# Kernel tuning notes

Measured on AMD Instinct MI355X. Metric: run time of the kernel, lower is better.

The kernel has to match this reference:

```python
import jax, jax.numpy as jnp
import numpy as np

B, IN = 8192, 8000
C, S, O = 16, 500, 64          # num_chunks, chunk_size, fc_repr_dim
F = C * O                       # fc_0_out_feat = 1024
E, D, T = 8, 512, 2            # num_experts, fc_task_dim, num_tasks
NC = (32, 2)                    # num_classes per task
EPS = 1e-5


def _bn(h, g, b, axis):
    # training-mode BatchNorm1d: biased variance over the batch axis
    m = h.mean(axis=axis, keepdims=True)
    v = h.var(axis=axis, keepdims=True)
    return (h - m) * jax.lax.rsqrt(v + EPS) * g + b


def _swish(x):
    return x * jax.nn.sigmoid(x)


def setup_inputs() -> dict:
    key = jax.random.key(0)
    ks = jax.random.split(key, 10)
    s = 0.02
    return {
        "x": jax.random.normal(ks[0], (B, IN), dtype=jnp.float32),
        "w0": jax.random.normal(ks[1], (C, O, S), dtype=jnp.float32) * s,
        "b0": jnp.zeros((F,), jnp.float32),
        "bn0_g": jnp.ones((F,), jnp.float32),
        "bn0_b": jnp.zeros((F,), jnp.float32),
        "gate_w": jax.random.normal(ks[2], (T, F, E), dtype=jnp.float32) * s,
        "gate_b": jnp.zeros((T, E), jnp.float32),
        "exp_w": jax.random.normal(ks[3], (E, F, D), dtype=jnp.float32) * s,
        "exp_bn_g": jnp.ones((E, D), jnp.float32),
        "exp_bn_b": jnp.zeros((E, D), jnp.float32),
        "task_w": jax.random.normal(ks[4], (T, D, D), dtype=jnp.float32) * s,
        "task_bn_g": jnp.ones((T, D), jnp.float32),
        "task_bn_b": jnp.zeros((T, D), jnp.float32),
        "fin_w_a": jax.random.normal(ks[5], (D, NC[0]), dtype=jnp.float32) * s,
        "fin_b_a": jnp.zeros((NC[0],), jnp.float32),
        "fin_w_b": jax.random.normal(ks[6], (D, NC[1]), dtype=jnp.float32) * s,
        "fin_b_b": jnp.zeros((NC[1],), jnp.float32),
    }


def reference(x, w0, b0, bn0_g, bn0_b, gate_w, gate_b, exp_w, exp_bn_g,
              exp_bn_b, task_w, task_bn_g, task_bn_b, fin_w_a, fin_b_a,
              fin_w_b, fin_b_b):
    b = x.shape[0]
    # SplitLinear: block-diagonal linear over C chunks of size S -> O each
    h0 = jnp.einsum('bcs,cos->bco', x.reshape(b, C, S), w0).reshape(b, F) + b0
    h0 = _swish(_bn(h0, bn0_g, bn0_b, axis=0))                  # [B, F]
    # per-task gates with softmax over experts
    gates = jax.nn.softmax(
        jnp.einsum('bf,tfe->tbe', h0, gate_w) + gate_b[:, None, :], axis=-1)
    # expert branches: Linear(no bias) + BN + Swish, vectorized over experts
    eh = jnp.einsum('bf,efd->bed', h0, exp_w)                   # [B, E, D]
    eh = _swish(_bn(eh, exp_bn_g, exp_bn_b, axis=0))
    # gate-weighted sum over experts, per task
    mix = jnp.einsum('tbe,bed->tbd', gates, eh)                 # [T, B, D]
    # task branches: Linear(no bias) + BN + Swish
    th = jnp.einsum('tbd,tdk->tbk', mix, task_w)
    th = _swish(_bn(th, task_bn_g[:, None, :], task_bn_b[:, None, :], axis=1))
    out_a = th[0] @ fin_w_a + fin_b_a                           # [B, 32]
    out_b = th[1] @ fin_w_b + fin_b_b                           # [B, 2]
    return jnp.concatenate([out_a, out_b], axis=1)             # [B, 34]
```

## Files before the change

### kernel.cpp

```cpp
#include <hip/hip_runtime.h>
#include <math.h>

#define B_ 8192
#define IN_ 8000
#define C_ 16
#define S_ 500
#define O_ 64
#define F_ 1024
#define E_ 8
#define D_ 512
#define T_ 2
#define OUTW 34
#define EPS_ 1e-5f

typedef __attribute__((ext_vector_type(8))) short bf16x8;
typedef __attribute__((ext_vector_type(4))) float f32x4;

__device__ __forceinline__ float swishf(float x) {
    return x / (1.0f + __expf(-x));
}

__device__ __forceinline__ unsigned short f2bf(float f) {
    union { float f; unsigned u; } c;
    c.f = f;
    unsigned r = c.u + 0x7fffu + ((c.u >> 16) & 1u);
    return (unsigned short)(r >> 16);
}
__device__ __forceinline__ float bf2f(unsigned short b) {
    union { unsigned u; float f; } c;
    c.u = ((unsigned)b) << 16;
    return c.f;
}

__device__ __forceinline__ void gld16(const void* g, void* l) {
    __builtin_amdgcn_global_load_lds(
        (const __attribute__((address_space(1))) void*)g,
        (__attribute__((address_space(3))) void*)l, 16, 0, 0);
}

__global__ __launch_bounds__(256) void k_split(const float* __restrict__ x,
                                               const float* __restrict__ w0,
                                               const float* __restrict__ b0,
                                               unsigned short* __restrict__ h0raw,
                                               float* __restrict__ psum,
                                               float* __restrict__ psq) {
    __shared__ __align__(16) unsigned short As[128 * 72];
    __shared__ __align__(16) unsigned short Bs[64 * 72];
    int tid = threadIdx.x;
    int c = blockIdx.y;
    int brow0 = blockIdx.x * 128;
    const float* xp = x + (size_t)brow0 * IN_ + c * S_;
    const float* wp = w0 + (size_t)c * O_ * S_;

    int w = tid >> 6, lane = tid & 63;
    int l15 = lane & 15, quad = lane >> 4;
    int wm = w * 32;

    f32x4 acc[2][4] = {};

    for (int k0 = 0; k0 < 512; k0 += 64) {
#pragma unroll
        for (int i = 0; i < 8; i++) {
            int li = tid + i * 256;
            int row = li >> 4, c4 = li & 15;
            int gk = k0 + c4 * 4;
            float4 v = make_float4(0.f, 0.f, 0.f, 0.f);
            if (gk + 3 < S_) v = *(const float4*)(xp + (size_t)row * IN_ + gk);
            unsigned short u[4] = { f2bf(v.x), f2bf(v.y), f2bf(v.z), f2bf(v.w) };
            *(ushort4*)&As[row * 72 + c4 * 4] = *(ushort4*)u;
        }
#pragma unroll
        for (int i = 0; i < 4; i++) {
            int li = tid + i * 256;
            int row = li >> 4, c4 = li & 15;
            int gk = k0 + c4 * 4;
            float4 v = make_float4(0.f, 0.f, 0.f, 0.f);
            if (gk + 3 < S_) v = *(const float4*)(wp + (size_t)row * S_ + gk);
            unsigned short u[4] = { f2bf(v.x), f2bf(v.y), f2bf(v.z), f2bf(v.w) };
            *(ushort4*)&Bs[row * 72 + c4 * 4] = *(ushort4*)u;
        }
        __syncthreads();
#pragma unroll
        for (int kk = 0; kk < 64; kk += 32) {
            bf16x8 af[2], wf[4];
#pragma unroll
            for (int i = 0; i < 2; i++)
                af[i] = *(const bf16x8*)&As[(wm + i * 16 + l15) * 72 + kk + quad * 8];
#pragma unroll
            for (int j = 0; j < 4; j++)
                wf[j] = *(const bf16x8*)&Bs[(j * 16 + l15) * 72 + kk + quad * 8];
#pragma unroll
            for (int i = 0; i < 2; i++)
#pragma unroll
                for (int j = 0; j < 4; j++)
                    acc[i][j] = __builtin_amdgcn_mfma_f32_16x16x32_bf16(af[i], wf[j], acc[i][j], 0, 0, 0);
        }
        __syncthreads();
    }

    int colbase = c * O_;
    float sj[4], qj[4];
#pragma unroll
    for (int j = 0; j < 4; j++) {
        int col = j * 16 + l15;
        float bb = b0[colbase + col];
        float s = 0.f, q = 0.f;
#pragma unroll
        for (int i = 0; i < 2; i++) {
#pragma unroll
            for (int reg = 0; reg < 4; reg++) {
                float v = acc[i][j][reg] + bb;
                int rl = wm + i * 16 + quad * 4 + reg;
                h0raw[(size_t)(brow0 + rl) * F_ + colbase + col] = f2bf(v);
                s += v; q += v * v;
            }
        }
        s += __shfl_down(s, 32, 64); s += __shfl_down(s, 16, 64);
        q += __shfl_down(q, 32, 64); q += __shfl_down(q, 16, 64);
        sj[j] = s; qj[j] = q;
    }
    __syncthreads();
    float* red = (float*)As;
    if (lane < 16) {
#pragma unroll
        for (int j = 0; j < 4; j++) {
            int col = j * 16 + l15;
            red[col * 4 + w] = sj[j];
            red[256 + col * 4 + w] = qj[j];
        }
    }
    __syncthreads();
    if (tid < 64) {
        float ss = red[tid * 4] + red[tid * 4 + 1] + red[tid * 4 + 2] + red[tid * 4 + 3];
        float qq = red[256 + tid * 4] + red[256 + tid * 4 + 1] + red[256 + tid * 4 + 2] + red[256 + tid * 4 + 3];
        size_t idx = (size_t)blockIdx.x * F_ + colbase + tid;
        psum[idx] = ss; psq[idx] = qq;
    }
}

__global__ __launch_bounds__(64) void k_stats_b(const float* __restrict__ psum,
                                                const float* __restrict__ psq,
                                                int N, int YS,
                                                const float* __restrict__ g,
                                                const float* __restrict__ beta,
                                                unsigned long long gslab,
                                                float* __restrict__ scale,
                                                float* __restrict__ shift,
                                                unsigned long long oslab) {
    int n = blockIdx.x * 64 + threadIdx.x;
    int z = blockIdx.z;
    float s = 0.f, q = 0.f;
    for (int y = 0; y < YS; y++) {
        size_t idx = ((size_t)(z * YS + y)) * N + n;
        s += psum[idx]; q += psq[idx];
    }
    float mean = s * (1.0f / B_);
    float var = q * (1.0f / B_) - mean * mean;
    float sc = g[z * gslab + n] * rsqrtf(var + EPS_);
    scale[z * oslab + n] = sc;
    shift[z * oslab + n] = beta[z * gslab + n] - mean * sc;
}

__global__ __launch_bounds__(256) void k_wt(const float* __restrict__ in,
                                            unsigned short* __restrict__ out,
                                            int K, int N) {
    __shared__ float t[32][33];
    int k0 = blockIdx.x * 32, n0 = blockIdx.y * 32, z = blockIdx.z;
    const float* ip = in + (size_t)z * K * N;
    unsigned short* op = out + (size_t)z * N * K;
    int tn = threadIdx.x & 31, tk = threadIdx.x >> 5;
#pragma unroll
    for (int p = 0; p < 4; p++) {
        int k = tk + p * 8;
        t[k][tn] = ip[(size_t)(k0 + k) * N + n0 + tn];
    }
    __syncthreads();
    int tk2 = threadIdx.x & 31, tn2 = threadIdx.x >> 5;
#pragma unroll
    for (int p = 0; p < 4; p++) {
        int n = tn2 + p * 8;
        op[(size_t)(n0 + n) * K + k0 + tk2] = f2bf(t[tk2][n]);
    }
}

__global__ __launch_bounds__(256) void k_bnswish_gates(const unsigned short* __restrict__ h0,
                                                       const float* __restrict__ scale,
                                                       const float* __restrict__ shift,
                                                       const float* __restrict__ gate_w,
                                                       const float* __restrict__ gate_b,
                                                       unsigned short* __restrict__ h0bf,
                                                       float* __restrict__ gates) {
    int b = blockIdx.x, tid = threadIdx.x;
    float part[16];
#pragma unroll
    for (int i = 0; i < 16; i++) part[i] = 0.f;
    const unsigned short* row = h0 + (size_t)b * F_;
    unsigned short* ob = h0bf + (size_t)b * F_;
#pragma unroll
    for (int it = 0; it < 4; it++) {
        int f = tid + it * 256;
        float v = bf2f(row[f]);
        float hv = scale[f] * v + shift[f];
        float sw = swishf(hv);
        ob[f] = f2bf(sw);
        const float* gw0 = gate_w + (size_t)f * E_;
        const float* gw1 = gate_w + (size_t)(F_ * E_) + (size_t)f * E_;
#pragma unroll
        for (int e = 0; e < E_; e++) part[e] += sw * gw0[e];
#pragma unroll
        for (int e = 0; e < E_; e++) part[8 + e] += sw * gw1[e];
    }
#pragma unroll
    for (int i = 0; i < 16; i++) {
        float v = part[i];
        for (int off = 32; off > 0; off >>= 1) v += __shfl_down(v, off, 64);
        part[i] = v;
    }
    __shared__ float red[4][16];
    __shared__ float gfin[16];
    int wave = tid >> 6, lane = tid & 63;
    if (lane == 0) {
#pragma unroll
        for (int i = 0; i < 16; i++) red[wave][i] = part[i];
    }
    __syncthreads();
    if (tid < 16) {
        float v = red[0][tid] + red[1][tid] + red[2][tid] + red[3][tid];
        int t = tid >> 3, e = tid & 7;
        gfin[tid] = v + gate_b[t * E_ + e];
    }
    __syncthreads();
    if (tid < 2) {
        float mx = -1e30f;
#pragma unroll
        for (int e = 0; e < 8; e++) mx = fmaxf(mx, gfin[tid * 8 + e]);
        float ex[8], sum = 0.f;
#pragma unroll
        for (int e = 0; e < 8; e++) { ex[e] = __expf(gfin[tid * 8 + e] - mx); sum += ex[e]; }
        float inv = 1.0f / sum;
#pragma unroll
        for (int e = 0; e < 8; e++)
            gates[(size_t)tid * (B_ * E_) + (size_t)b * E_ + e] = ex[e] * inv;
    }
}

__global__ __launch_bounds__(256) void k_gemm_bf16(const unsigned short* __restrict__ A,
                                                   unsigned long long aslab,
                                                   const unsigned short* __restrict__ Wt,
                                                   unsigned long long wslab,
                                                   unsigned short* __restrict__ C,
                                                   unsigned long long cslab, int K,
                                                   float* __restrict__ psum,
                                                   float* __restrict__ psq) {
    __shared__ __align__(16) unsigned short As[128 * 32];
    __shared__ __align__(16) unsigned short Ws[128 * 32];
    int z = blockIdx.z;
    A  += (size_t)z * aslab;
    Wt += (size_t)z * wslab;
    C  += (size_t)z * cslab;
    const int N = gridDim.y * 128;
    int row0 = blockIdx.x * 128, col0 = blockIdx.y * 128;
    int tid = threadIdx.x;
    int w = tid >> 6, lane = tid & 63;
    int l15 = lane & 15, quad = lane >> 4;

    const unsigned short* ga0 = A  + (size_t)(row0 + w * 32 + (lane >> 2)) * K + (lane & 3) * 8;
    const unsigned short* ga1 = ga0 + 16 * (size_t)K;
    const unsigned short* gw0 = Wt + (size_t)(col0 + w * 32 + (lane >> 2)) * K + (lane & 3) * 8;
    const unsigned short* gw1 = gw0 + 16 * (size_t)K;
    unsigned short* la0 = As + (w * 32) * 32;
    unsigned short* la1 = As + (w * 32 + 16) * 32;
    unsigned short* lw0 = Ws + (w * 32) * 32;
    unsigned short* lw1 = Ws + (w * 32 + 16) * 32;

    int wm = (w & 1) * 64, wn = (w >> 1) * 64;
    const unsigned short* Afr = As + (size_t)(wm + l15) * 32 + quad * 8;
    const unsigned short* Wfr = Ws + (size_t)(wn + l15) * 32 + quad * 8;

    f32x4 acc[4][4] = {};

    for (int k0 = 0; k0 < K; k0 += 32) {
        gld16(ga0 + k0, la0);
        gld16(ga1 + k0, la1);
        gld16(gw0 + k0, lw0);
        gld16(gw1 + k0, lw1);
        __syncthreads();
        bf16x8 af[4], wf[4];
#pragma unroll
        for (int i = 0; i < 4; i++) af[i] = *(const bf16x8*)(Afr + i * 16 * 32);
#pragma unroll
        for (int j = 0; j < 4; j++) wf[j] = *(const bf16x8*)(Wfr + j * 16 * 32);
#pragma unroll
        for (int i = 0; i < 4; i++)
#pragma unroll
            for (int j = 0; j < 4; j++)
                acc[i][j] = __builtin_amdgcn_mfma_f32_16x16x32_bf16(af[i], wf[j], acc[i][j], 0, 0, 0);
        __syncthreads();
    }

#pragma unroll
    for (int i = 0; i < 4; i++) {
        int r = row0 + wm + i * 16 + quad * 4;
#pragma unroll
        for (int j = 0; j < 4; j++) {
            int cc = col0 + wn + j * 16 + l15;
            unsigned short* cp = C + (size_t)r * N + cc;
#pragma unroll
            for (int reg = 0; reg < 4; reg++)
                cp[(size_t)reg * N] = f2bf(acc[i][j][reg]);
        }
    }

    float* red = (float*)As;
    float sj[4], qj[4];
#pragma unroll
    for (int j = 0; j < 4; j++) {
        float s = 0.f, q = 0.f;
#pragma unroll
        for (int i = 0; i < 4; i++)
#pragma unroll
            for (int reg = 0; reg < 4; reg++) {
                float v = acc[i][j][reg];
                s += v; q += v * v;
            }
        s += __shfl_down(s, 32, 64); s += __shfl_down(s, 16, 64);
        q += __shfl_down(q, 32, 64); q += __shfl_down(q, 16, 64);
        sj[j] = s; qj[j] = q;
    }
    if (lane < 16) {
#pragma unroll
        for (int j = 0; j < 4; j++) {
            int cib = wn + j * 16 + lane;
            red[cib * 2 + (w & 1)] = sj[j];
            red[256 + cib * 2 + (w & 1)] = qj[j];
        }
    }
    __syncthreads();
    if (tid < 128) {
        float s = red[tid * 2] + red[tid * 2 + 1];
        float q = red[256 + tid * 2] + red[256 + tid * 2 + 1];
        size_t row = (size_t)z * gridDim.x + blockIdx.x;
        psum[row * N + col0 + tid] = s;
        psq[row * N + col0 + tid] = q;
    }
}

__global__ __launch_bounds__(256) void k_mix(const unsigned short* __restrict__ eh,
                                             const float* __restrict__ scale,
                                             const float* __restrict__ shift,
                                             const float* __restrict__ gates,
                                             unsigned short* __restrict__ mix) {
    __shared__ float scl[E_ * D_], shl[E_ * D_];
    __shared__ float gl[2][2][8];
    int tid = threadIdx.x;
#pragma unroll
    for (int i = 0; i < 4; i++) {
        int li = tid + i * 256;
        ((float4*)scl)[li] = ((const float4*)scale)[li];
        ((float4*)shl)[li] = ((const float4*)shift)[li];
    }
    if (tid < 32) {
        int sub = tid >> 4, t = (tid >> 3) & 1, e = tid & 7;
        gl[sub][t][e] = gates[(size_t)t * (B_ * E_) + (size_t)(blockIdx.x * 2 + sub) * E_ + e];
    }
    __syncthreads();
    int sub = tid >> 7;
    int b = blockIdx.x * 2 + sub;
    int d0 = (tid & 127) * 4;
    float a0[4] = {0.f, 0.f, 0.f, 0.f}, a1[4] = {0.f, 0.f, 0.f, 0.f};
#pragma unroll
    for (int e = 0; e < E_; e++) {
        ushort4 u = *(const ushort4*)&eh[(size_t)b * (E_ * D_) + e * D_ + d0];
        float4 sc4 = *(const float4*)&scl[e * D_ + d0];
        float4 sh4 = *(const float4*)&shl[e * D_ + d0];
        float g0 = gl[sub][0][e], g1 = gl[sub][1][e];
        unsigned short uu[4] = { u.x, u.y, u.z, u.w };
        float scv[4] = { sc4.x, sc4.y, sc4.z, sc4.w };
        float shv[4] = { sh4.x, sh4.y, sh4.z, sh4.w };
#pragma unroll
        for (int l = 0; l < 4; l++) {
            float sw = swishf(scv[l] * bf2f(uu[l]) + shv[l]);
            a0[l] += g0 * sw;
            a1[l] += g1 * sw;
        }
    }
    unsigned short o0[4], o1[4];
#pragma unroll
    for (int l = 0; l < 4; l++) { o0[l] = f2bf(a0[l]); o1[l] = f2bf(a1[l]); }
    *(ushort4*)&mix[(size_t)b * D_ + d0] = *(ushort4*)o0;
    *(ushort4*)&mix[(size_t)(B_ * D_) + (size_t)b * D_ + d0] = *(ushort4*)o1;
}

__global__ __launch_bounds__(256) void k_final(const unsigned short* __restrict__ th,
                                               const float* __restrict__ scale,
                                               const float* __restrict__ shift,
                                               const float* __restrict__ fwa,
                                               const float* __restrict__ fba,
                                               const float* __restrict__ fwb,
                                               const float* __restrict__ fbb,
                                               float* __restrict__ out) {
    __shared__ float t0[8][D_], t1[8][D_];
    __shared__ float pb[64];
    int tid = threadIdx.x;
    int b0 = blockIdx.x * 8;
#pragma unroll
    for (int t = 0; t < 2; t++) {
#pragma unroll
        for (int i = 0; i < 4; i++) {
            int li = tid + i * 256;
            int row = li >> 7, d = (li & 127) * 4;
            ushort4 u = *(const ushort4*)&th[((size_t)t * B_ + b0 + row) * D_ + d];
            unsigned short uu[4] = { u.x, u.y, u.z, u.w };
            float* dst = t ? &t1[row][d] : &t0[row][d];
#pragma unroll
            for (int l = 0; l < 4; l++)
                dst[l] = swishf(scale[t * D_ + d + l] * bf2f(uu[l]) + shift[t * D_ + d + l]);
        }
    }
    __syncthreads();
    {
        int row = tid >> 5, col = tid & 31;
        float acc = fba[col];
        for (int d = 0; d < D_; d++) acc += t0[row][d] * fwa[d * 32 + col];
        out[(size_t)(b0 + row) * OUTW + col] = acc;
    }
    if (tid < 64) {
        int row = tid >> 3, colb = (tid >> 2) & 1, part = tid & 3;
        float a = 0.f;
        for (int d = part * 128; d < part * 128 + 128; d++) a += t1[row][d] * fwb[d * 2 + colb];
        pb[tid] = a;
    }
    __syncthreads();
    if (tid < 16) {
        int row = tid >> 1, colb = tid & 1;
        int base = row * 8 + colb * 4;
        float a = fbb[colb] + pb[base] + pb[base + 1] + pb[base + 2] + pb[base + 3];
        out[(size_t)(b0 + row) * OUTW + 32 + colb] = a;
    }
}

extern "C" void kernel_launch(void* const* d_in, const int* in_sizes, int n_in,
                              void* d_out, int out_size, void* d_ws, size_t ws_size,
                              hipStream_t stream) {
    const float* x        = (const float*)d_in[0];
    const float* w0       = (const float*)d_in[1];
    const float* b0       = (const float*)d_in[2];
    const float* bn0_g    = (const float*)d_in[3];
    const float* bn0_b    = (const float*)d_in[4];
    const float* gate_w   = (const float*)d_in[5];
    const float* gate_b   = (const float*)d_in[6];
    const float* exp_w    = (const float*)d_in[7];
    const float* exp_bn_g = (const float*)d_in[8];
    const float* exp_bn_b = (const float*)d_in[9];
    const float* task_w   = (const float*)d_in[10];
    const float* task_bn_g= (const float*)d_in[11];
    const float* task_bn_b= (const float*)d_in[12];
    const float* fwa      = (const float*)d_in[13];
    const float* fba      = (const float*)d_in[14];
    const float* fwb      = (const float*)d_in[15];
    const float* fbb      = (const float*)d_in[16];
    float* out = (float*)d_out;

    float* ws = (float*)d_ws;
    unsigned short* ehbf  = (unsigned short*)ws;
    unsigned short* h0raw = (unsigned short*)(ws + 16777216);
    unsigned short* thbf  = ehbf;
    unsigned short* mixbf = h0raw;
    unsigned short* h0bf  = (unsigned short*)(ws + 20971520);
    unsigned short* wtE   = (unsigned short*)(ws + 25165824);
    unsigned short* twt   = (unsigned short*)(ws + 27262976);
    float* gates = ws + 27525120;
    float* sc0   = ws + 27656192;
    float* sh0   = sc0 + 1024;
    float* scE   = sh0 + 1024;
    float* shE   = scE + 4096;
    float* scT   = shE + 4096;
    float* shT   = scT + 1024;
    float* psum  = shT + 1024;
    float* psq   = psum + 262144;

    k_wt<<<dim3(32, 16, 8), 256, 0, stream>>>(exp_w, wtE, F_, D_);
    k_wt<<<dim3(16, 16, 2), 256, 0, stream>>>(task_w, twt, D_, D_);
    k_split<<<dim3(64, 16), 256, 0, stream>>>(x, w0, b0, h0raw, psum, psq);
    k_stats_b<<<dim3(16, 1, 1), 64, 0, stream>>>(psum, psq, F_, 64, bn0_g, bn0_b, 0ull, sc0, sh0, 0ull);
    k_bnswish_gates<<<dim3(B_), 256, 0, stream>>>(h0raw, sc0, sh0, gate_w, gate_b, h0bf, gates);
    k_gemm_bf16<<<dim3(64, 32, 1), 256, 0, stream>>>(h0bf, 0ull, wtE, 0ull, ehbf, 0ull, F_, psum, psq);
    k_stats_b<<<dim3(64, 1, 1), 64, 0, stream>>>(psum, psq, E_ * D_, 64, exp_bn_g, exp_bn_b, 0ull, scE, shE, 0ull);
    k_mix<<<dim3(B_ / 2), 256, 0, stream>>>(ehbf, scE, shE, gates, mixbf);
    k_gemm_bf16<<<dim3(64, 4, 2), 256, 0, stream>>>(mixbf, (unsigned long long)(B_ * D_),
                                                    twt, (unsigned long long)(D_ * D_),
                                                    thbf, (unsigned long long)(B_ * D_), D_,
                                                    psum, psq);
    k_stats_b<<<dim3(8, 1, 2), 64, 0, stream>>>(psum, psq, D_, 64, task_bn_g, task_bn_b, 512ull, scT, shT, 512ull);
    k_final<<<dim3(B_ / 8), 256, 0, stream>>>(thbf, scT, shT, fwa, fba, fwb, fbb, out);
}
```

Baseline: 689.9 us.

## Add 256x256-tile ping-pong MFMA GEMM for expert projection and vectorize bnswish

Replaces the expert GEMM (8192x4096x1024) with a new 512-thread kernel that computes 256x256 output tiles. It double-buffers LDS loads, raises wave priority around MFMA phases, swizzles block order for cache locality, and fuses BN partial statistics at the new row-block granularity (32 partials). It also vectorizes the bnswish/gates kernel loads and stores to 4-wide. The goal is more data reuse per tile and fewer global loads, at the cost of heavy register pressure and only 512 blocks.

```diff
diff --git a/kernel.cpp b/kernel.cpp
--- a/kernel.cpp
+++ b/kernel.cpp
@@ -196,20 +196,26 @@
     for (int i = 0; i < 16; i++) part[i] = 0.f;
     const unsigned short* row = h0 + (size_t)b * F_;
     unsigned short* ob = h0bf + (size_t)b * F_;
-#pragma unroll
-    for (int it = 0; it < 4; it++) {
-        int f = tid + it * 256;
-        float v = bf2f(row[f]);
-        float hv = scale[f] * v + shift[f];
-        float sw = swishf(hv);
-        ob[f] = f2bf(sw);
-        const float* gw0 = gate_w + (size_t)f * E_;
-        const float* gw1 = gate_w + (size_t)(F_ * E_) + (size_t)f * E_;
+    int f0 = tid * 4;
+    ushort4 u = *(const ushort4*)(row + f0);
+    float4 sc4 = *(const float4*)(scale + f0);
+    float4 sh4 = *(const float4*)(shift + f0);
+    unsigned short uu[4] = { u.x, u.y, u.z, u.w };
+    float scv[4] = { sc4.x, sc4.y, sc4.z, sc4.w };
+    float shv[4] = { sh4.x, sh4.y, sh4.z, sh4.w };
+    unsigned short ov[4];
+#pragma unroll
+    for (int j = 0; j < 4; j++) {
+        float sw = swishf(scv[j] * bf2f(uu[j]) + shv[j]);
+        ov[j] = f2bf(sw);
+        const float* gw0 = gate_w + (size_t)(f0 + j) * E_;
+        const float* gw1 = gw0 + (size_t)F_ * E_;
 #pragma unroll
         for (int e = 0; e < E_; e++) part[e] += sw * gw0[e];
 #pragma unroll
         for (int e = 0; e < E_; e++) part[8 + e] += sw * gw1[e];
     }
+    *(ushort4*)(ob + f0) = *(ushort4*)ov;
 #pragma unroll
     for (int i = 0; i < 16; i++) {
         float v = part[i];
@@ -342,6 +348,172 @@
         size_t row = (size_t)z * gridDim.x + blockIdx.x;
         psum[row * N + col0 + tid] = s;
         psq[row * N + col0 + tid] = q;
+    }
+}
+
+__global__ __launch_bounds__(512, 2) void k_gemm256(const unsigned short* __restrict__ A,
+                                                    const unsigned short* __restrict__ Wt,
+                                                    unsigned short* __restrict__ Cc,
+                                                    int N, int K,
+                                                    float* __restrict__ psum,
+                                                    float* __restrict__ psq) {
+    __shared__ __align__(16) unsigned short lds[2][2][2][8192];
+    int tid = threadIdx.x;
+    int w = tid >> 6, lane = tid & 63;
+    int l15 = lane & 15, quad = lane >> 4;
+    int wm = w >> 2, wn = w & 3;
+
+    int lin = blockIdx.y * gridDim.x + blockIdx.x;
+    int cpx = (gridDim.x * gridDim.y) >> 3;
+    int swz = (lin & 7) * cpx + (lin >> 3);
+    int bx = swz & (gridDim.x - 1), by = swz / gridDim.x;
+    int row0 = bx * 256, col0 = by * 256;
+
+    int srow = tid >> 3, sperm = (tid & 7) ^ (srow & 7);
+    const unsigned short* pA = A  + (size_t)(row0 + srow) * K + sperm * 8;
+    const unsigned short* pB = Wt + (size_t)(col0 + srow) * K + sperm * 8;
+
+    int aoffs[2];
+#pragma unroll
+    for (int kk = 0; kk < 2; kk++)
+        aoffs[kk] = l15 * 64 + ((kk * 4 + quad) ^ (l15 & 7)) * 8;
+
+    f32x4 acc[8][4] = {};
+    bf16x8 afr[4][2], bfr[2][2];
+    int nt = K >> 6;
+
+#define STAGE256(t1, nb) do {                                                              \
+    const unsigned short* sA = pA + (size_t)(t1) * 64;                                     \
+    const unsigned short* sB = pB + (size_t)(t1) * 64;                                     \
+    _Pragma("unroll")                                                                      \
+    for (int h = 0; h < 2; h++)                                                            \
+        _Pragma("unroll")                                                                  \
+        for (int L = 0; L < 2; L++) {                                                      \
+            gld16(sA + (size_t)(h * 128 + L * 64) * K, &lds[nb][0][h][w * 512 + L * 4096]);\
+            gld16(sB + (size_t)(h * 128 + L * 64) * K, &lds[nb][1][h][w * 512 + L * 4096]);\
+        }                                                                                  \
+} while (0)
+
+#define LDA256(mh) do {                                                                    \
+    _Pragma("unroll")                                                                      \
+    for (int mf = 0; mf < 4; mf++)                                                         \
+        _Pragma("unroll")                                                                  \
+        for (int kk = 0; kk < 2; kk++)                                                     \
+            afr[mf][kk] = *(const bf16x8*)(Ab + ((mh) * 4 + mf) * 1024 + aoffs[kk]);       \
+} while (0)
+
+#define LDB256(nh) do {                                                                    \
+    _Pragma("unroll")                                                                      \
+    for (int nf = 0; nf < 2; nf++)                                                         \
+        _Pragma("unroll")                                                                  \
+        for (int kk = 0; kk < 2; kk++)                                                     \
+            bfr[nf][kk] = *(const bf16x8*)(Bb + ((nh) * 2 + nf) * 1024 + aoffs[kk]);       \
+} while (0)
+
+#define MMA256(mh, nh) do {                                                                \
+    _Pragma("unroll")                                                                      \
+    for (int mf = 0; mf < 4; mf++)                                                         \
+        _Pragma("unroll")                                                                  \
+        for (int nf = 0; nf < 2; nf++)                                                     \
+            _Pragma("unroll")                                                              \
+            for (int kk = 0; kk < 2; kk++)                                                 \
+                acc[(mh) * 4 + mf][(nh) * 2 + nf] = __builtin_amdgcn_mfma_f32_16x16x32_bf16(\
+                    afr[mf][kk], bfr[nf][kk], acc[(mh) * 4 + mf][(nh) * 2 + nf], 0, 0, 0); \
+} while (0)
+
+#define PHASE_MID()                                                                        \
+    __builtin_amdgcn_s_barrier();                                                          \
+    asm volatile("s_waitcnt lgkmcnt(0)" ::: "memory");                                     \
+    __builtin_amdgcn_sched_barrier(0);                                                     \
+    __builtin_amdgcn_s_setprio(1);
+
+#define PHASE_END()                                                                        \
+    __builtin_amdgcn_s_setprio(0);                                                         \
+    __builtin_amdgcn_sched_barrier(0);                                                     \
+    __builtin_amdgcn_s_barrier();
+
+    STAGE256(0, 0);
+    asm volatile("s_waitcnt vmcnt(0)" ::: "memory");
+    __builtin_amdgcn_s_barrier();
+
+    for (int t = 0; t < nt; t++) {
+        int buf = t & 1;
+        const unsigned short* Ab = &lds[buf][0][wm][0];
+        const unsigned short* Bb = &lds[buf][1][wn >> 1][(wn & 1) * 4096];
+        LDA256(0); LDB256(0);
+        if (t + 1 < nt) STAGE256(t + 1, buf ^ 1);
+        PHASE_MID();
+        MMA256(0, 0);
+        PHASE_END();
+        LDB256(1);
+        PHASE_MID();
+        MMA256(0, 1);
+        PHASE_END();
+        LDA256(1);
+        PHASE_MID();
+        MMA256(1, 1);
+        PHASE_END();
+        LDB256(0);
+        PHASE_MID();
+        MMA256(1, 0);
+        __builtin_amdgcn_s_setprio(0);
+        __builtin_amdgcn_sched_barrier(0);
+        asm volatile("s_waitcnt vmcnt(0)" ::: "memory");
+        __builtin_amdgcn_s_barrier();
+    }
+#undef STAGE256
+#undef LDA256
+#undef LDB256
+#undef MMA256
+#undef PHASE_MID
+#undef PHASE_END
+
+    __syncthreads();
+
+#pragma unroll
+    for (int mf = 0; mf < 8; mf++) {
+        int r = row0 + wm * 128 + mf * 16 + quad * 4;
+#pragma unroll
+        for (int nf = 0; nf < 4; nf++) {
+            int cc = col0 + wn * 64 + nf * 16 + l15;
+            unsigned short* cp = Cc + (size_t)r * N + cc;
+#pragma unroll
+            for (int reg = 0; reg < 4; reg++)
+                cp[(size_t)reg * N] = f2bf(acc[mf][nf][reg]);
+        }
+    }
+
+    float* red = (float*)&lds[0][0][0][0];
+    float* redq = red + 512;
+    float sj[4], qj[4];
+#pragma unroll
+    for (int nf = 0; nf < 4; nf++) {
+        float s = 0.f, q = 0.f;
+#pragma unroll
+        for (int mf = 0; mf < 8; mf++)
+#pragma unroll
+            for (int reg = 0; reg < 4; reg++) {
+                float v = acc[mf][nf][reg];
+                s += v; q += v * v;
+            }
+        s += __shfl_down(s, 32, 64); s += __shfl_down(s, 16, 64);
+        q += __shfl_down(q, 32, 64); q += __shfl_down(q, 16, 64);
+        sj[nf] = s; qj[nf] = q;
+    }
+    if (quad == 0) {
+#pragma unroll
+        for (int nf = 0; nf < 4; nf++) {
+            int cib = wn * 64 + nf * 16 + l15;
+            red[cib * 2 + wm] = sj[nf];
+            redq[cib * 2 + wm] = qj[nf];
+        }
+    }
+    __syncthreads();
+    if (tid < 256) {
+        float s = red[tid * 2] + red[tid * 2 + 1];
+        float q = redq[tid * 2] + redq[tid * 2 + 1];
+        psum[(size_t)bx * N + col0 + tid] = s;
+        psq [(size_t)bx * N + col0 + tid] = q;
     }
 }
 
@@ -484,8 +656,8 @@
     k_split<<<dim3(64, 16), 256, 0, stream>>>(x, w0, b0, h0raw, psum, psq);
     k_stats_b<<<dim3(16, 1, 1), 64, 0, stream>>>(psum, psq, F_, 64, bn0_g, bn0_b, 0ull, sc0, sh0, 0ull);
     k_bnswish_gates<<<dim3(B_), 256, 0, stream>>>(h0raw, sc0, sh0, gate_w, gate_b, h0bf, gates);
-    k_gemm_bf16<<<dim3(64, 32, 1), 256, 0, stream>>>(h0bf, 0ull, wtE, 0ull, ehbf, 0ull, F_, psum, psq);
-    k_stats_b<<<dim3(64, 1, 1), 64, 0, stream>>>(psum, psq, E_ * D_, 64, exp_bn_g, exp_bn_b, 0ull, scE, shE, 0ull);
+    k_gemm256<<<dim3(32, 16), 512, 0, stream>>>(h0bf, wtE, ehbf, E_ * D_, F_, psum, psq);
+    k_stats_b<<<dim3(64, 1, 1), 64, 0, stream>>>(psum, psq, E_ * D_, 32, exp_bn_g, exp_bn_b, 0ull, scE, shE, 0ull);
     k_mix<<<dim3(B_ / 2), 256, 0, stream>>>(ehbf, scE, shE, gates, mixbf);
     k_gemm_bf16<<<dim3(64, 4, 2), 256, 0, stream>>>(mixbf, (unsigned long long)(B_ * D_),
                                                     twt, (unsigned long long)(D_ * D_),
```

Measured after the change: 687.9 us. About the same (-0.3%).
